# Optimization experiments

Hardware: AMD Instinct MI355X
Metric: run time of the kernel (lower is better)

Reference implementation:

```python
import jax, jax.numpy as jnp
import numpy as np

NT, NV, ND, NM, NP = 50000, 1000, 20000, 5000, 8000
E = 100000
D, H, C = 256, 4, 64          # gnn_hidden_dim, heads, per-head channels
TS_FEAT, EMB, L = 64, 128, 2
NEG_SLOPE = 0.2

SIZES = {'ts': NT, 'vital': NV, 'diag': ND, 'med': NM, 'proc': NP}
EDGE_TYPES = [('ts', 'vital'), ('vital', 'ts'), ('ts', 'diag'), ('diag', 'ts'),
              ('ts', 'med'), ('med', 'ts'), ('ts', 'proc'), ('proc', 'ts')]
T = len(EDGE_TYPES)


def setup_inputs():
    key = jax.random.key(0)
    ks = jax.random.split(key, 32)
    def nrm(k, shape, s=0.05):
        return jax.random.normal(k, shape, dtype=jnp.float32) * s
    inp = {}
    inp['ts_x'] = nrm(ks[0], (NT, TS_FEAT), 1.0)
    inp['emb_vital'] = nrm(ks[1], (NV, EMB), 1.0)
    inp['emb_diag'] = nrm(ks[2], (ND, EMB), 1.0)
    inp['emb_med'] = nrm(ks[3], (NM, EMB), 1.0)
    inp['emb_proc'] = nrm(ks[4], (NP, EMB), 1.0)
    inp['Wp_ts'] = nrm(ks[5], (TS_FEAT, D)); inp['bp_ts'] = jnp.zeros((D,), jnp.float32)
    inp['Wp_c'] = nrm(ks[6], (4, EMB, D)); inp['bp_c'] = jnp.zeros((4, D), jnp.float32)
    inp['Wsrc'] = nrm(ks[7], (L, T, D, H * C))
    inp['Wdst'] = nrm(ks[8], (L, T, D, H * C))
    inp['asrc'] = nrm(ks[9], (L, T, H, C))
    inp['adst'] = nrm(ks[10], (L, T, H, C))
    inp['bconv'] = jnp.zeros((L, T, H * C), jnp.float32)
    inp['Wc1'] = nrm(ks[11], (D, D // 2)); inp['bc1'] = jnp.zeros((D // 2,), jnp.float32)
    inp['Wc2'] = nrm(ks[12], (D // 2, 1)); inp['bc2'] = jnp.zeros((1,), jnp.float32)
    names = ['ei_tv', 'ei_vt', 'ei_td', 'ei_dt', 'ei_tm', 'ei_mt', 'ei_tp', 'ei_pt']
    for i, ((s, d), nm) in enumerate(zip(EDGE_TYPES, names)):
        k1, k2 = jax.random.split(ks[13 + i])
        src = jax.random.randint(k1, (E,), 0, SIZES[s], dtype=jnp.int32)
        dst = jax.random.randint(k2, (E,), 0, SIZES[d], dtype=jnp.int32)
        inp[nm] = jnp.stack([src, dst])
    return inp


def gat_conv(xs, xd, Ws, Wd, a_s, a_d, b, ei, nd):
    """Bipartite PyG GATConv: add_self_loops=False, concat heads, eval (no dropout)."""
    hs = (xs @ Ws).reshape(-1, H, C)            # [Ns,H,C]
    hd = (xd @ Wd).reshape(-1, H, C)            # [Nd,H,C]
    es = jnp.sum(hs * a_s, axis=-1)             # [Ns,H]
    ed = jnp.sum(hd * a_d, axis=-1)             # [Nd,H]
    src, dst = ei[0], ei[1]
    e = jax.nn.leaky_relu(es[src] + ed[dst], NEG_SLOPE)   # [E,H]
    m = jax.ops.segment_max(e, dst, num_segments=nd)      # segment softmax over dst
    ex = jnp.exp(e - m[dst])
    den = jax.ops.segment_sum(ex, dst, num_segments=nd)
    alpha = ex / (den[dst] + 1e-16)
    msg = (alpha[:, :, None] * hs[src]).reshape(-1, H * C)  # [E,H*C]
    return jax.ops.segment_sum(msg, dst, num_segments=nd) + b


def _forward(ts_x, emb_vital, emb_diag, emb_med, emb_proc, Wp_ts, bp_ts, Wp_c, bp_c,
             Wsrc, Wdst, asrc, adst, bconv, Wc1, bc1, Wc2, bc2, edges):
    x = {'ts': ts_x @ Wp_ts + bp_ts,
         'vital': emb_vital @ Wp_c[0] + bp_c[0],
         'diag': emb_diag @ Wp_c[1] + bp_c[1],
         'med': emb_med @ Wp_c[2] + bp_c[2],
         'proc': emb_proc @ Wp_c[3] + bp_c[3]}
    for l in range(L):
        new = {k: jnp.zeros((SIZES[k], D), jnp.float32) for k in x}  # HeteroConv aggr='sum'
        for t, ((s, d), ei) in enumerate(zip(EDGE_TYPES, edges)):
            new[d] = new[d] + gat_conv(x[s], x[d], Wsrc[l, t], Wdst[l, t],
                                       asrc[l, t], adst[l, t], bconv[l, t], ei, SIZES[d])
        x = {k: jax.nn.relu(v) for k, v in new.items()}
    g = jnp.mean(x['ts'], axis=0)               # graph embedding
    h = jax.nn.relu(g @ Wc1 + bc1)
    logits = h @ Wc2 + bc2
    return jnp.squeeze(logits, -1)              # output_classes == 1 -> scalar


def reference(ts_x, emb_vital, emb_diag, emb_med, emb_proc, Wp_ts, bp_ts, Wp_c, bp_c,
              Wsrc, Wdst, asrc, adst, bconv, Wc1, bc1, Wc2, bc2,
              ei_tv, ei_vt, ei_td, ei_dt, ei_tm, ei_mt, ei_tp, ei_pt):
    edges = (ei_tv, ei_vt, ei_td, ei_dt, ei_tm, ei_mt, ei_tp, ei_pt)
    return _forward(ts_x, emb_vital, emb_diag, emb_med, emb_proc, Wp_ts, bp_ts, Wp_c, bp_c,
                    Wsrc, Wdst, asrc, adst, bconv, Wc1, bc1, Wc2, bc2, edges)
```

## Files before the change

kernel.cpp:

```cpp
#include <hip/hip_runtime.h>

#define E_N 100000
#define NTOT 84000
#define NDST 234000

typedef __attribute__((ext_vector_type(8))) short bfrag8;
typedef __attribute__((ext_vector_type(4))) float accf4;

__device__ __forceinline__ void atomAddF(float* p, float v) {
    unsafeAtomicAdd(p, v);
}

__device__ __forceinline__ float lrelu(float v) { return v >= 0.f ? v : 0.2f * v; }

__device__ __forceinline__ unsigned short f2bf(float f) {
    unsigned u = __float_as_uint(f);
    return (unsigned short)((u + 0x7FFFu + ((u >> 16) & 1u)) >> 16);
}
__device__ __forceinline__ float bf2f(unsigned short h) {
    return __uint_as_float(((unsigned)h) << 16);
}

__constant__ int c_tbase[8] = {0, 1000, 51000, 71000, 121000, 126000, 176000, 184000};

struct EI8 { const int* p[8]; };

struct BTJob { const float* W; unsigned short* hi; unsigned short* lo; int K; int kshift; };
struct BTBatch { BTJob j[17]; };

__global__ __launch_bounds__(256) void makeBT(BTBatch b)
{
    BTJob jb = b.j[blockIdx.z];
    int idx = blockIdx.x * 256 + threadIdx.x;
    if (idx >= (jb.K << 8)) return;
    int n = idx >> jb.kshift;
    int k = idx & (jb.K - 1);
    float w = jb.W[(size_t)k * 256 + n];
    unsigned short h = f2bf(w);
    jb.hi[idx] = h;
    jb.lo[idx] = f2bf(w - bf2f(h));
}

struct MJob { const float* A; const unsigned short* BThi; const unsigned short* BTlo;
              float* C; unsigned short* Cbf; const float* bias; int M; int K; int relu; };
struct MBatch { MJob j[8]; };

__global__ __launch_bounds__(256, 2) void gemm_mfma(MBatch batch)
{
    const MJob jb = batch.j[blockIdx.z];
    const int bm = blockIdx.x * 128;
    if (bm >= jb.M) return;
    const int bn = blockIdx.y * 128;
    const int M = jb.M, K = jb.K;

    __shared__ unsigned short Ah[128 * 40];
    __shared__ unsigned short Al[128 * 40];
    __shared__ unsigned short B1[128 * 40];
    __shared__ unsigned short B2[128 * 40];

    const int tid  = threadIdx.x;
    const int wv   = tid >> 6;
    const int lane = tid & 63;
    const int qr = wv >> 1, qc = wv & 1;
    const int lm = lane & 15;
    const int lq = lane >> 4;

    accf4 acc[4][4] = {};

    for (int k0 = 0; k0 < K; k0 += 32) {
#pragma unroll
        for (int it = 0; it < 4; ++it) {
            int slot = it * 256 + tid;
            int m  = slot >> 3;
            int kq = (slot & 7) << 2;
            float4 v = make_float4(0.f, 0.f, 0.f, 0.f);
            if (bm + m < M) v = *(const float4*)(jb.A + (size_t)(bm + m) * K + k0 + kq);
            int o = m * 40 + kq;
            unsigned short h0 = f2bf(v.x), h1 = f2bf(v.y), h2 = f2bf(v.z), h3 = f2bf(v.w);
            Ah[o + 0] = h0; Ah[o + 1] = h1; Ah[o + 2] = h2; Ah[o + 3] = h3;
            Al[o + 0] = f2bf(v.x - bf2f(h0));
            Al[o + 1] = f2bf(v.y - bf2f(h1));
            Al[o + 2] = f2bf(v.z - bf2f(h2));
            Al[o + 3] = f2bf(v.w - bf2f(h3));
        }
#pragma unroll
        for (int it = 0; it < 2; ++it) {
            int slot = it * 256 + tid;
            int n  = slot >> 2;
            int kq = (slot & 3) << 3;
            size_t go = (size_t)(bn + n) * K + k0 + kq;
            *(uint4*)&B1[n * 40 + kq] = *(const uint4*)(jb.BThi + go);
            *(uint4*)&B2[n * 40 + kq] = *(const uint4*)(jb.BTlo + go);
        }
        __syncthreads();

        bfrag8 ah[4], al[4], b1[4], b2[4];
#pragma unroll
        for (int t = 0; t < 4; ++t) {
            int am  = qr * 64 + t * 16 + lm;
            int bnn = qc * 64 + t * 16 + lm;
            ah[t] = *(const bfrag8*)&Ah[am * 40 + lq * 8];
            al[t] = *(const bfrag8*)&Al[am * 40 + lq * 8];
            b1[t] = *(const bfrag8*)&B1[bnn * 40 + lq * 8];
            b2[t] = *(const bfrag8*)&B2[bnn * 40 + lq * 8];
        }
#pragma unroll
        for (int mt = 0; mt < 4; ++mt)
#pragma unroll
            for (int nt = 0; nt < 4; ++nt) {
                acc[mt][nt] = __builtin_amdgcn_mfma_f32_16x16x32_bf16(ah[mt], b1[nt], acc[mt][nt], 0, 0, 0);
                acc[mt][nt] = __builtin_amdgcn_mfma_f32_16x16x32_bf16(al[mt], b1[nt], acc[mt][nt], 0, 0, 0);
                acc[mt][nt] = __builtin_amdgcn_mfma_f32_16x16x32_bf16(ah[mt], b2[nt], acc[mt][nt], 0, 0, 0);
            }
        __syncthreads();
    }

#pragma unroll
    for (int nt = 0; nt < 4; ++nt) {
        int col = bn + qc * 64 + nt * 16 + lm;
        float bv = jb.bias ? jb.bias[col] : 0.f;
#pragma unroll
        for (int mt = 0; mt < 4; ++mt) {
            int row0 = bm + qr * 64 + mt * 16 + lq * 4;
#pragma unroll
            for (int r = 0; r < 4; ++r) {
                int row = row0 + r;
                if (row < M) {
                    float o = acc[mt][nt][r] + bv;
                    if (jb.relu) o = fmaxf(o, 0.f);
                    if (jb.C)   jb.C[(size_t)row * 256 + col] = o;
                    if (jb.Cbf) jb.Cbf[(size_t)row * 256 + col] = f2bf(o);
                }
            }
        }
    }
}

__global__ __launch_bounds__(256) void fill_weff(const float* __restrict__ Wsrc,
                                                 const float* __restrict__ Wdst,
                                                 const float* __restrict__ asrc,
                                                 const float* __restrict__ adst,
                                                 float* __restrict__ weff)
{
    int idx = blockIdx.x * 256 + threadIdx.x;
    if (idx >= 81920) return;
    int col = idx & 31;
    int k   = (idx >> 5) & 255;
    int lnt = idx >> 13;
    int nt  = lnt % 5;
    int l   = lnt / 5;
    bool is_src; int t, h;
    if (nt == 0) {
        if (col < 16) { is_src = true;  t = (col >> 2) * 2;            h = col & 3; }
        else          { is_src = false; t = ((col - 16) >> 2) * 2 + 1; h = col & 3; }
    } else {
        if (col < 4)      { is_src = true;  t = 2 * nt - 1; h = col; }
        else if (col < 8) { is_src = false; t = 2 * nt - 2; h = col - 4; }
        else { weff[idx] = 0.f; return; }
    }
    const float* W = (is_src ? Wsrc : Wdst) + ((size_t)((l * 8 + t) * 256 + k)) * 256 + h * 64;
    const float* a = (is_src ? asrc : adst) + ((size_t)((l * 8 + t) * 4 + h)) * 64;
    float val = 0.f;
    for (int c = 0; c < 64; c++) val += W[c] * a[c];
    weff[idx] = val;
}

template<int NO>
__device__ __forceinline__ void attnproj_body(const float* __restrict__ xrow,
                                              const float* __restrict__ W,
                                              float* __restrict__ out)
{
    float acc[NO];
#pragma unroll
    for (int j = 0; j < NO; j++) acc[j] = 0.f;
    for (int k = 0; k < 256; k += 4) {
        const float4 xv = *(const float4*)(xrow + k);
#pragma unroll
        for (int j = 0; j < NO; j++) {
            acc[j] += xv.x * W[(k + 0) * 32 + j] + xv.y * W[(k + 1) * 32 + j]
                    + xv.z * W[(k + 2) * 32 + j] + xv.w * W[(k + 3) * 32 + j];
        }
    }
#pragma unroll
    for (int j = 0; j < NO; j++) out[j] = acc[j];
}

__global__ __launch_bounds__(256) void attnproj(const float* __restrict__ x,
                                                const float* __restrict__ weff_l,
                                                float* __restrict__ attnT,
                                                float* __restrict__ attnC)
{
    int n = blockIdx.x * 256 + threadIdx.x;
    if (n >= NTOT) return;
    if (n < 50000) {
        attnproj_body<32>(x + (size_t)n * 256, weff_l, attnT + (size_t)n * 32);
    } else {
        int nt = (n < 51000) ? 1 : (n < 71000) ? 2 : (n < 76000) ? 3 : 4;
        attnproj_body<8>(x + (size_t)n * 256, weff_l + nt * 8192, attnC + (size_t)(n - 50000) * 8);
    }
}

__global__ __launch_bounds__(256) void count_k(EI8 ei, int* __restrict__ cnt)
{
    int g = blockIdx.x * 256 + threadIdx.x;
    if (g >= 8 * E_N) return;
    int t = g / E_N;
    int i = g - t * E_N;
    int d = ei.p[t][E_N + i];
    atomicAdd(&cnt[c_tbase[t] + d], 1);
}

__global__ __launch_bounds__(256) void scanA(const int* __restrict__ cnt,
                                             int* __restrict__ rowptr,
                                             int* __restrict__ bsum)
{
    __shared__ int sd[256];
    int b = blockIdx.x, t = threadIdx.x;
    int base = b * 1024 + t * 4;
    int v0 = 0, v1 = 0, v2 = 0, v3 = 0;
    if (base + 0 < NDST) v0 = cnt[base + 0];
    if (base + 1 < NDST) v1 = cnt[base + 1];
    if (base + 2 < NDST) v2 = cnt[base + 2];
    if (base + 3 < NDST) v3 = cnt[base + 3];
    int s = v0 + v1 + v2 + v3;
    sd[t] = s;
    __syncthreads();
    for (int off = 1; off < 256; off <<= 1) {
        int x = 0;
        if (t >= off) x = sd[t - off];
        __syncthreads();
        if (t >= off) sd[t] += x;
        __syncthreads();
    }
    int run = sd[t] - s;
    if (t == 255) bsum[b] = sd[255];
    if (base + 0 < NDST) rowptr[base + 0] = run;          run += v0;
    if (base + 1 < NDST) rowptr[base + 1] = run;          run += v1;
    if (base + 2 < NDST) rowptr[base + 2] = run;          run += v2;
    if (base + 3 < NDST) rowptr[base + 3] = run;
}

__global__ __launch_bounds__(256) void scanB(int* __restrict__ bsum, int nb)
{
    __shared__ int sd[256];
    int t = threadIdx.x;
    int v = (t < nb) ? bsum[t] : 0;
    sd[t] = v;
    __syncthreads();
    for (int off = 1; off < 256; off <<= 1) {
        int x = 0;
        if (t >= off) x = sd[t - off];
        __syncthreads();
        if (t >= off) sd[t] += x;
        __syncthreads();
    }
    if (t < nb) bsum[t] = sd[t] - v;
}

__global__ __launch_bounds__(256) void scanC(int* __restrict__ rowptr,
                                             const int* __restrict__ bsum,
                                             int* __restrict__ cursor)
{
    int b = blockIdx.x, t = threadIdx.x;
    int off = bsum[b];
    int base = b * 1024 + t * 4;
#pragma unroll
    for (int j = 0; j < 4; j++) {
        int i = base + j;
        if (i < NDST) {
            int r = rowptr[i] + off;
            rowptr[i] = r;
            cursor[i] = r;
        }
    }
    if (b == 0 && t == 0) rowptr[NDST] = 8 * E_N;
}

__global__ __launch_bounds__(256) void place_k(EI8 ei, int* __restrict__ cursor,
                                               int* __restrict__ ssrc)
{
    int g = blockIdx.x * 256 + threadIdx.x;
    if (g >= 8 * E_N) return;
    int t = g / E_N;
    int i = g - t * E_N;
    int d = ei.p[t][E_N + i];
    int s = ei.p[t][i];
    int pos = atomicAdd(&cursor[c_tbase[t] + d], 1);
    ssrc[pos] = s;
}

__global__ __launch_bounds__(256) void aggx_k(const float* __restrict__ attnT,
                                              const float* __restrict__ attnC,
                                              const unsigned short* __restrict__ xtsbf,
                                              const int* __restrict__ rowptr,
                                              const int* __restrict__ ssrc,
                                              float* __restrict__ aggx)
{
    int w = blockIdx.x * 4 + (threadIdx.x >> 6);
    int lane = threadIdx.x & 63;
    int h = lane >> 4;
    int ch = (h << 6) | ((lane & 15) << 2);
    int q, dloc;
    if (w < 1000)       { q = 0; dloc = w; }
    else if (w < 21000) { q = 1; dloc = w - 1000; }
    else if (w < 26000) { q = 2; dloc = w - 21000; }
    else                { q = 3; dloc = w - 26000; }
    const int csr4[4]  = {0, 51000, 121000, 176000};
    const int soff4[4] = {0, 4, 8, 12};
    int soff = soff4[q];
    int r0 = rowptr[csr4[q] + dloc], r1 = rowptr[csr4[q] + dloc + 1];
    float ed = attnC[(size_t)w * 8 + 4 + h];
    float den = 0.f, sx = 0.f, sy = 0.f, sz = 0.f, sw = 0.f;
    int e = r0;
    for (; e + 4 <= r1; e += 4) {
        int sA = ssrc[e], sB = ssrc[e + 1], sC = ssrc[e + 2], sD = ssrc[e + 3];
        float eA = attnT[(size_t)sA * 32 + soff + h];
        float eB = attnT[(size_t)sB * 32 + soff + h];
        float eC = attnT[(size_t)sC * 32 + soff + h];
        float eD = attnT[(size_t)sD * 32 + soff + h];
        ushort4 rA = *(const ushort4*)(xtsbf + (size_t)sA * 256 + ch);
        ushort4 rB = *(const ushort4*)(xtsbf + (size_t)sB * 256 + ch);
        ushort4 rC = *(const ushort4*)(xtsbf + (size_t)sC * 256 + ch);
        ushort4 rD = *(const ushort4*)(xtsbf + (size_t)sD * 256 + ch);
        float xA = __expf(lrelu(eA + ed));
        float xB = __expf(lrelu(eB + ed));
        float xC = __expf(lrelu(eC + ed));
        float xD = __expf(lrelu(eD + ed));
        den += (xA + xB) + (xC + xD);
        sx += xA * bf2f(rA.x) + xB * bf2f(rB.x) + xC * bf2f(rC.x) + xD * bf2f(rD.x);
        sy += xA * bf2f(rA.y) + xB * bf2f(rB.y) + xC * bf2f(rC.y) + xD * bf2f(rD.y);
        sz += xA * bf2f(rA.z) + xB * bf2f(rB.z) + xC * bf2f(rC.z) + xD * bf2f(rD.z);
        sw += xA * bf2f(rA.w) + xB * bf2f(rB.w) + xC * bf2f(rC.w) + xD * bf2f(rD.w);
    }
    for (; e < r1; e++) {
        int s = ssrc[e];
        float es = attnT[(size_t)s * 32 + soff + h];
        float ex = __expf(lrelu(es + ed));
        den += ex;
        ushort4 rv = *(const ushort4*)(xtsbf + (size_t)s * 256 + ch);
        sx += ex * bf2f(rv.x); sy += ex * bf2f(rv.y);
        sz += ex * bf2f(rv.z); sw += ex * bf2f(rv.w);
    }
    float inv = 1.f / (den + 1e-16f);
    float4 o; o.x = sx * inv; o.y = sy * inv; o.z = sz * inv; o.w = sw * inv;
    *(float4*)(aggx + (size_t)w * 256 + ch) = o;
}

__global__ __launch_bounds__(256) void agg_ts(const float* __restrict__ attnT,
                                              const float* __restrict__ attnC,
                                              const unsigned short* __restrict__ hscbf,
                                              const int* __restrict__ rowptr,
                                              const int* __restrict__ ssrc,
                                              const float* __restrict__ bconv_l,
                                              float* __restrict__ xout)
{
    int d = blockIdx.x * 4 + (threadIdx.x >> 6);
    int lane = threadIdx.x & 63;
    int h = lane >> 4;
    int ch = (h << 6) | ((lane & 15) << 2);
    const int co4[4]   = {0, 1000, 21000, 26000};
    const int tb4[4]   = {1000, 71000, 126000, 184000};
    const int doff4[4] = {16, 20, 24, 28};
    const int bo4[4]   = {256, 768, 1280, 1792};

    int r0q[4], nq[4]; float edq[4];
    int mx = 0;
#pragma unroll
    for (int q = 0; q < 4; q++) {
        int a = rowptr[tb4[q] + d], b = rowptr[tb4[q] + d + 1];
        r0q[q] = a; nq[q] = b - a;
        mx = max(mx, b - a);
        edq[q] = attnT[(size_t)d * 32 + doff4[q] + h];
    }
    float den[4] = {0.f, 0.f, 0.f, 0.f};
    float sx[4] = {0.f, 0.f, 0.f, 0.f}, sy[4] = {0.f, 0.f, 0.f, 0.f};
    float sz[4] = {0.f, 0.f, 0.f, 0.f}, sw[4] = {0.f, 0.f, 0.f, 0.f};
    for (int i = 0; i < mx; i++) {
#pragma unroll
        for (int q = 0; q < 4; q++) {
            if (i < nq[q]) {
                int s = ssrc[r0q[q] + i];
                float es = attnC[(size_t)(co4[q] + s) * 8 + h];
                float ex = __expf(lrelu(es + edq[q]));
                den[q] += ex;
                ushort4 hv = *(const ushort4*)(hscbf + (size_t)(co4[q] + s) * 256 + ch);
                sx[q] += ex * bf2f(hv.x); sy[q] += ex * bf2f(hv.y);
                sz[q] += ex * bf2f(hv.z); sw[q] += ex * bf2f(hv.w);
            }
        }
    }
    float ax = 0.f, ay = 0.f, az = 0.f, aw = 0.f;
#pragma unroll
    for (int q = 0; q < 4; q++) {
        const float* b = bconv_l + bo4[q] + ch;
        float inv = 1.f / (den[q] + 1e-16f);
        ax += b[0] + sx[q] * inv; ay += b[1] + sy[q] * inv;
        az += b[2] + sz[q] * inv; aw += b[3] + sw[q] * inv;
    }
    float4 o;
    o.x = fmaxf(ax, 0.f); o.y = fmaxf(ay, 0.f);
    o.z = fmaxf(az, 0.f); o.w = fmaxf(aw, 0.f);
    *(float4*)(xout + (size_t)d * 256 + ch) = o;
}

__global__ __launch_bounds__(256) void colsum_ts(const float* __restrict__ x,
                                                 float* __restrict__ gsum)
{
    int c = threadIdx.x;
    float s = 0.f;
    for (int r = blockIdx.x; r < 50000; r += gridDim.x) s += x[(size_t)r * 256 + c];
    atomAddF(gsum + c, s);
}

__global__ __launch_bounds__(128) void head_k(const float* __restrict__ gsum,
                                              const float* __restrict__ Wc1,
                                              const float* __restrict__ bc1,
                                              const float* __restrict__ Wc2,
                                              const float* __restrict__ bc2,
                                              float* __restrict__ out)
{
    __shared__ float g[256];
    __shared__ float red[128];
    int t = threadIdx.x;
    g[t] = gsum[t] * (1.f / 50000.f);
    g[t + 128] = gsum[t + 128] * (1.f / 50000.f);
    __syncthreads();
    float acc = bc1[t];
    for (int k = 0; k < 256; k++) acc += g[k] * Wc1[k * 128 + t];
    red[t] = fmaxf(acc, 0.f) * Wc2[t];
    __syncthreads();
    for (int sft = 64; sft > 0; sft >>= 1) {
        if (t < sft) red[t] += red[t + sft];
        __syncthreads();
    }
    if (t == 0) out[0] = red[0] + bc2[0];
}

extern "C" void kernel_launch(void* const* d_in, const int* in_sizes, int n_in,
                              void* d_out, int out_size, void* d_ws, size_t ws_size,
                              hipStream_t stream)
{
    const float* ts_x   = (const float*)d_in[0];
    const float* emb[4] = {(const float*)d_in[1], (const float*)d_in[2],
                           (const float*)d_in[3], (const float*)d_in[4]};
    const float* Wp_ts  = (const float*)d_in[5];
    const float* bp_ts  = (const float*)d_in[6];
    const float* Wp_c   = (const float*)d_in[7];
    const float* bp_c   = (const float*)d_in[8];
    const float* Wsrc   = (const float*)d_in[9];
    const float* Wdst   = (const float*)d_in[10];
    const float* asrc   = (const float*)d_in[11];
    const float* adst   = (const float*)d_in[12];
    const float* bconv  = (const float*)d_in[13];
    const float* Wc1    = (const float*)d_in[14];
    const float* bc1    = (const float*)d_in[15];
    const float* Wc2    = (const float*)d_in[16];
    const float* bc2    = (const float*)d_in[17];
    EI8 ei;
    for (int t = 0; t < 8; t++) ei.p[t] = (const int*)d_in[18 + t];

    float* x0    = (float*)d_ws;
    float* x1    = x0    + 21504000;
    float* attnT = x1    + 21504000;
    float* attnC = attnT + 1600000;
    float* weff  = attnC + 272000;
    float* gsum  = weff  + 81920;
    int* rowptr  = (int*)(gsum + 256);
    int* bsum    = rowptr + 234004;
    int* ssrc    = bsum + 256;
    unsigned short* xtsbf = (unsigned short*)(ssrc + 800000);
    unsigned short* hscbf = xtsbf + 12800000;
    unsigned short* btp   = hscbf + 8704000;
    int* cursor  = (int*)hscbf;
    float* aggx  = x1;

    unsigned short* bt_ts_h = btp;
    unsigned short* bt_ts_l = bt_ts_h + 16384;
    unsigned short* bt_c_h[4], *bt_c_l[4];
    {
        unsigned short* p = bt_ts_l + 16384;
        for (int q = 0; q < 4; q++) { bt_c_h[q] = p; p += 32768; bt_c_l[q] = p; p += 32768; }
    }
    unsigned short* bt_w = bt_ts_l + 16384 + 8 * 32768;
    auto wpan_h = [&](int l, int t) { return bt_w + (size_t)((l == 0 ? t : 8 + t / 2) * 2) * 65536; };
    auto wpan_l = [&](int l, int t) { return wpan_h(l, t) + 65536; };

    hipMemsetAsync(cursor, 0, NDST * sizeof(int), stream);
    count_k<<<3125, 256, 0, stream>>>(ei, cursor);
    scanA<<<229, 256, 0, stream>>>(cursor, rowptr, bsum);
    scanB<<<1, 256, 0, stream>>>(bsum, 229);
    scanC<<<229, 256, 0, stream>>>(rowptr, bsum, cursor);
    place_k<<<3125, 256, 0, stream>>>(ei, cursor, ssrc);

    {
        BTBatch b = {};
        int zi = 0;
        b.j[zi++] = {Wp_ts, bt_ts_h, bt_ts_l, 64, 6};
        for (int q = 0; q < 4; q++)
            b.j[zi++] = {Wp_c + q * 32768, bt_c_h[q], bt_c_l[q], 128, 7};
        for (int t = 0; t < 8; t++)
            b.j[zi++] = {Wsrc + (size_t)(0 * 8 + t) * 65536, wpan_h(0, t), wpan_l(0, t), 256, 8};
        for (int t = 1; t < 8; t += 2)
            b.j[zi++] = {Wsrc + (size_t)(1 * 8 + t) * 65536, wpan_h(1, t), wpan_l(1, t), 256, 8};
        makeBT<<<dim3(256, 1, 17), 256, 0, stream>>>(b);
    }

    fill_weff<<<320, 256, 0, stream>>>(Wsrc, Wdst, asrc, adst, weff);

    static const int Nd4[4]    = {1000, 20000, 5000, 8000};
    static const int co4[4]    = {0, 1000, 21000, 26000};
    static const int dbase4[4] = {50000, 51000, 71000, 76000};
    static const int tsrc[4]   = {1, 3, 5, 7};
    static const int tdst[4]   = {0, 2, 4, 6};

    {
        MBatch b = {};
        b.j[0] = {ts_x, bt_ts_h, bt_ts_l, x0, xtsbf, bp_ts, 50000, 64, 0};
        for (int q = 0; q < 4; q++)
            b.j[1 + q] = {emb[q], bt_c_h[q], bt_c_l[q], x0 + (size_t)dbase4[q] * 256,
                          nullptr, bp_c + q * 256, Nd4[q], 128, 0};
        gemm_mfma<<<dim3(391, 2, 5), 256, 0, stream>>>(b);
    }

    attnproj<<<329, 256, 0, stream>>>(x0, weff, attnT, attnC);
    aggx_k<<<8500, 256, 0, stream>>>(attnT, attnC, xtsbf, rowptr, ssrc, aggx);
    {
        MBatch b = {};
        for (int q = 0; q < 4; q++)
            b.j[q] = {x0 + (size_t)dbase4[q] * 256, wpan_h(0, tsrc[q]), wpan_l(0, tsrc[q]),
                      nullptr, hscbf + (size_t)co4[q] * 256, nullptr, Nd4[q], 256, 0};
        for (int q = 0; q < 4; q++)
            b.j[4 + q] = {aggx + (size_t)co4[q] * 256, wpan_h(0, tdst[q]), wpan_l(0, tdst[q]),
                          x1 + (size_t)dbase4[q] * 256, nullptr, bconv + tdst[q] * 256, Nd4[q], 256, 1};
        gemm_mfma<<<dim3(157, 2, 8), 256, 0, stream>>>(b);
    }
    agg_ts<<<12500, 256, 0, stream>>>(attnT, attnC, hscbf, rowptr, ssrc, bconv, x1);

    attnproj<<<329, 256, 0, stream>>>(x1, weff + 40960, attnT, attnC);
    {
        MBatch b = {};
        for (int q = 0; q < 4; q++)
            b.j[q] = {x1 + (size_t)dbase4[q] * 256, wpan_h(1, tsrc[q]), wpan_l(1, tsrc[q]),
                      nullptr, hscbf + (size_t)co4[q] * 256, nullptr, Nd4[q], 256, 0};
        gemm_mfma<<<dim3(157, 2, 4), 256, 0, stream>>>(b);
    }
    agg_ts<<<12500, 256, 0, stream>>>(attnT, attnC, hscbf, rowptr, ssrc, bconv + 2048, x0);

    hipMemsetAsync(gsum, 0, 256 * sizeof(float), stream);
    colsum_ts<<<256, 256, 0, stream>>>(x0, gsum);
    head_k<<<1, 128, 0, stream>>>(gsum, Wc1, bc1, Wc2, bc2, (float*)d_out);
}
```

Measured before the change: 756.7 us.

## Store activations as packed hi/lo bf16, swizzle GEMM LDS, fuse final aggregation with column sum

Activations are now stored as packed hi/lo bf16 pairs in 32-bit words, so GEMMs reading them skip the per-tile fp32 split and conversion. The GEMM LDS layout drops the padding in favour of an XOR swizzle, which frees shared memory, and occupancy is raised to 4 blocks per SM. The last-layer ts aggregation is fused with the column mean reduction, so the 50000x256 output is never written and re-read. The packed format keeps roughly fp32 precision but adds pack/unpack ALU work, and the fused kernel serializes 8 destinations per wave with fewer blocks.

```diff
diff --git a/kernel.cpp b/kernel.cpp
--- a/kernel.cpp
+++ b/kernel.cpp
@@ -19,6 +19,14 @@
 }
 __device__ __forceinline__ float bf2f(unsigned short h) {
     return __uint_as_float(((unsigned)h) << 16);
+}
+__device__ __forceinline__ unsigned packf(float o) {
+    unsigned short h = f2bf(o);
+    unsigned short l = f2bf(o - bf2f(h));
+    return (unsigned)h | ((unsigned)l << 16);
+}
+__device__ __forceinline__ float unpk(unsigned u) {
+    return __uint_as_float(u << 16) + __uint_as_float(u & 0xffff0000u);
 }
 
 __constant__ int c_tbase[8] = {0, 1000, 51000, 71000, 121000, 126000, 176000, 184000};
@@ -41,11 +49,11 @@
     jb.lo[idx] = f2bf(w - bf2f(h));
 }
 
-struct MJob { const float* A; const unsigned short* BThi; const unsigned short* BTlo;
-              float* C; unsigned short* Cbf; const float* bias; int M; int K; int relu; };
+struct MJob { const void* A; const unsigned short* BThi; const unsigned short* BTlo;
+              unsigned* Cp; unsigned short* Cbf; const float* bias; int M; int K; int relu; int af32; };
 struct MBatch { MJob j[8]; };
 
-__global__ __launch_bounds__(256, 2) void gemm_mfma(MBatch batch)
+__global__ __launch_bounds__(256, 4) void gemm_mfma(MBatch batch)
 {
     const MJob jb = batch.j[blockIdx.z];
     const int bm = blockIdx.x * 128;
@@ -53,10 +61,10 @@
     const int bn = blockIdx.y * 128;
     const int M = jb.M, K = jb.K;
 
-    __shared__ unsigned short Ah[128 * 40];
-    __shared__ unsigned short Al[128 * 40];
-    __shared__ unsigned short B1[128 * 40];
-    __shared__ unsigned short B2[128 * 40];
+    __shared__ unsigned short Ah[128 * 32];
+    __shared__ unsigned short Al[128 * 32];
+    __shared__ unsigned short B1[128 * 32];
+    __shared__ unsigned short B2[128 * 32];
 
     const int tid  = threadIdx.x;
     const int wv   = tid >> 6;
@@ -73,24 +81,39 @@
             int slot = it * 256 + tid;
             int m  = slot >> 3;
             int kq = (slot & 7) << 2;
-            float4 v = make_float4(0.f, 0.f, 0.f, 0.f);
-            if (bm + m < M) v = *(const float4*)(jb.A + (size_t)(bm + m) * K + k0 + kq);
-            int o = m * 40 + kq;
-            unsigned short h0 = f2bf(v.x), h1 = f2bf(v.y), h2 = f2bf(v.z), h3 = f2bf(v.w);
-            Ah[o + 0] = h0; Ah[o + 1] = h1; Ah[o + 2] = h2; Ah[o + 3] = h3;
-            Al[o + 0] = f2bf(v.x - bf2f(h0));
-            Al[o + 1] = f2bf(v.y - bf2f(h1));
-            Al[o + 2] = f2bf(v.z - bf2f(h2));
-            Al[o + 3] = f2bf(v.w - bf2f(h3));
+            unsigned h01, h23, l01, l23;
+            if (jb.af32) {
+                float4 v = make_float4(0.f, 0.f, 0.f, 0.f);
+                if (bm + m < M) v = *(const float4*)((const float*)jb.A + (size_t)(bm + m) * K + k0 + kq);
+                unsigned short h0 = f2bf(v.x), h1 = f2bf(v.y), h2 = f2bf(v.z), h3 = f2bf(v.w);
+                unsigned short l0 = f2bf(v.x - bf2f(h0)), l1 = f2bf(v.y - bf2f(h1));
+                unsigned short l2 = f2bf(v.z - bf2f(h2)), l3 = f2bf(v.w - bf2f(h3));
+                h01 = (unsigned)h0 | ((unsigned)h1 << 16); h23 = (unsigned)h2 | ((unsigned)h3 << 16);
+                l01 = (unsigned)l0 | ((unsigned)l1 << 16); l23 = (unsigned)l2 | ((unsigned)l3 << 16);
+            } else {
+                uint4 v = make_uint4(0u, 0u, 0u, 0u);
+                if (bm + m < M) v = *(const uint4*)((const unsigned*)jb.A + (size_t)(bm + m) * K + k0 + kq);
+                h01 = (v.x & 0xffffu) | (v.y << 16);
+                h23 = (v.z & 0xffffu) | (v.w << 16);
+                l01 = (v.x >> 16) | (v.y & 0xffff0000u);
+                l23 = (v.z >> 16) | (v.w & 0xffff0000u);
+            }
+            int g = kq >> 3, half = (kq >> 2) & 1;
+            int off = m * 32 + ((g ^ (m & 3)) << 3) + half * 4;
+            uint2 hw; hw.x = h01; hw.y = h23;
+            uint2 lw; lw.x = l01; lw.y = l23;
+            *(uint2*)&Ah[off] = hw;
+            *(uint2*)&Al[off] = lw;
         }
 #pragma unroll
         for (int it = 0; it < 2; ++it) {
             int slot = it * 256 + tid;
-            int n  = slot >> 2;
-            int kq = (slot & 3) << 3;
-            size_t go = (size_t)(bn + n) * K + k0 + kq;
-            *(uint4*)&B1[n * 40 + kq] = *(const uint4*)(jb.BThi + go);
-            *(uint4*)&B2[n * 40 + kq] = *(const uint4*)(jb.BTlo + go);
+            int n = slot >> 2;
+            int g = slot & 3;
+            size_t go = (size_t)(bn + n) * K + k0 + g * 8;
+            int off = n * 32 + ((g ^ (n & 3)) << 3);
+            *(uint4*)&B1[off] = *(const uint4*)(jb.BThi + go);
+            *(uint4*)&B2[off] = *(const uint4*)(jb.BTlo + go);
         }
         __syncthreads();
 
@@ -99,10 +122,10 @@
         for (int t = 0; t < 4; ++t) {
             int am  = qr * 64 + t * 16 + lm;
             int bnn = qc * 64 + t * 16 + lm;
-            ah[t] = *(const bfrag8*)&Ah[am * 40 + lq * 8];
-            al[t] = *(const bfrag8*)&Al[am * 40 + lq * 8];
-            b1[t] = *(const bfrag8*)&B1[bnn * 40 + lq * 8];
-            b2[t] = *(const bfrag8*)&B2[bnn * 40 + lq * 8];
+            ah[t] = *(const bfrag8*)&Ah[am * 32 + ((lq ^ (am & 3)) << 3)];
+            al[t] = *(const bfrag8*)&Al[am * 32 + ((lq ^ (am & 3)) << 3)];
+            b1[t] = *(const bfrag8*)&B1[bnn * 32 + ((lq ^ (bnn & 3)) << 3)];
+            b2[t] = *(const bfrag8*)&B2[bnn * 32 + ((lq ^ (bnn & 3)) << 3)];
         }
 #pragma unroll
         for (int mt = 0; mt < 4; ++mt)
@@ -128,7 +151,7 @@
                 if (row < M) {
                     float o = acc[mt][nt][r] + bv;
                     if (jb.relu) o = fmaxf(o, 0.f);
-                    if (jb.C)   jb.C[(size_t)row * 256 + col] = o;
+                    if (jb.Cp)  jb.Cp[(size_t)row * 256 + col] = packf(o);
                     if (jb.Cbf) jb.Cbf[(size_t)row * 256 + col] = f2bf(o);
                 }
             }
@@ -166,7 +189,7 @@
 }
 
 template<int NO>
-__device__ __forceinline__ void attnproj_body(const float* __restrict__ xrow,
+__device__ __forceinline__ void attnproj_body(const unsigned* __restrict__ xrow,
                                               const float* __restrict__ W,
                                               float* __restrict__ out)
 {
@@ -174,18 +197,19 @@
 #pragma unroll
     for (int j = 0; j < NO; j++) acc[j] = 0.f;
     for (int k = 0; k < 256; k += 4) {
-        const float4 xv = *(const float4*)(xrow + k);
+        const uint4 xv = *(const uint4*)(xrow + k);
+        float x0 = unpk(xv.x), x1 = unpk(xv.y), x2 = unpk(xv.z), x3 = unpk(xv.w);
 #pragma unroll
         for (int j = 0; j < NO; j++) {
-            acc[j] += xv.x * W[(k + 0) * 32 + j] + xv.y * W[(k + 1) * 32 + j]
-                    + xv.z * W[(k + 2) * 32 + j] + xv.w * W[(k + 3) * 32 + j];
+            acc[j] += x0 * W[(k + 0) * 32 + j] + x1 * W[(k + 1) * 32 + j]
+                    + x2 * W[(k + 2) * 32 + j] + x3 * W[(k + 3) * 32 + j];
         }
     }
 #pragma unroll
     for (int j = 0; j < NO; j++) out[j] = acc[j];
 }
 
-__global__ __launch_bounds__(256) void attnproj(const float* __restrict__ x,
+__global__ __launch_bounds__(256) void attnproj(const unsigned* __restrict__ x,
                                                 const float* __restrict__ weff_l,
                                                 float* __restrict__ attnT,
                                                 float* __restrict__ attnC)
@@ -294,7 +318,7 @@
                                               const unsigned short* __restrict__ xtsbf,
                                               const int* __restrict__ rowptr,
                                               const int* __restrict__ ssrc,
-                                              float* __restrict__ aggx)
+                                              unsigned* __restrict__ aggx)
 {
     int w = blockIdx.x * 4 + (threadIdx.x >> 6);
     int lane = threadIdx.x & 63;
@@ -342,8 +366,10 @@
         sz += ex * bf2f(rv.z); sw += ex * bf2f(rv.w);
     }
     float inv = 1.f / (den + 1e-16f);
-    float4 o; o.x = sx * inv; o.y = sy * inv; o.z = sz * inv; o.w = sw * inv;
-    *(float4*)(aggx + (size_t)w * 256 + ch) = o;
+    uint4 o;
+    o.x = packf(sx * inv); o.y = packf(sy * inv);
+    o.z = packf(sz * inv); o.w = packf(sw * inv);
+    *(uint4*)(aggx + (size_t)w * 256 + ch) = o;
 }
 
 __global__ __launch_bounds__(256) void agg_ts(const float* __restrict__ attnT,
@@ -352,7 +378,7 @@
                                               const int* __restrict__ rowptr,
                                               const int* __restrict__ ssrc,
                                               const float* __restrict__ bconv_l,
-                                              float* __restrict__ xout)
+                                              unsigned* __restrict__ xout)
 {
     int d = blockIdx.x * 4 + (threadIdx.x >> 6);
     int lane = threadIdx.x & 63;
@@ -397,19 +423,83 @@
         ax += b[0] + sx[q] * inv; ay += b[1] + sy[q] * inv;
         az += b[2] + sz[q] * inv; aw += b[3] + sw[q] * inv;
     }
-    float4 o;
-    o.x = fmaxf(ax, 0.f); o.y = fmaxf(ay, 0.f);
-    o.z = fmaxf(az, 0.f); o.w = fmaxf(aw, 0.f);
-    *(float4*)(xout + (size_t)d * 256 + ch) = o;
-}
-
-__global__ __launch_bounds__(256) void colsum_ts(const float* __restrict__ x,
-                                                 float* __restrict__ gsum)
-{
-    int c = threadIdx.x;
-    float s = 0.f;
-    for (int r = blockIdx.x; r < 50000; r += gridDim.x) s += x[(size_t)r * 256 + c];
-    atomAddF(gsum + c, s);
+    uint4 o;
+    o.x = packf(fmaxf(ax, 0.f)); o.y = packf(fmaxf(ay, 0.f));
+    o.z = packf(fmaxf(az, 0.f)); o.w = packf(fmaxf(aw, 0.f));
+    *(uint4*)(xout + (size_t)d * 256 + ch) = o;
+}
+
+__global__ __launch_bounds__(256) void agg_tsum(const float* __restrict__ attnT,
+                                                const float* __restrict__ attnC,
+                                                const unsigned short* __restrict__ hscbf,
+                                                const int* __restrict__ rowptr,
+                                                const int* __restrict__ ssrc,
+                                                const float* __restrict__ bconv_l,
+                                                float* __restrict__ gsum)
+{
+    int wv = threadIdx.x >> 6, lane = threadIdx.x & 63;
+    int h = lane >> 4;
+    int ch = (h << 6) | ((lane & 15) << 2);
+    const int co4[4]   = {0, 1000, 21000, 26000};
+    const int tb4[4]   = {1000, 71000, 126000, 184000};
+    const int doff4[4] = {16, 20, 24, 28};
+    const int bo4[4]   = {256, 768, 1280, 1792};
+    float cs0 = 0.f, cs1 = 0.f, cs2 = 0.f, cs3 = 0.f;
+
+    for (int i8 = 0; i8 < 8; ++i8) {
+        int d = (blockIdx.x * 4 + wv) * 8 + i8;
+        if (d >= 50000) break;
+        int r0q[4], nq[4]; float edq[4];
+        int mx = 0;
+#pragma unroll
+        for (int q = 0; q < 4; q++) {
+            int a = rowptr[tb4[q] + d], b = rowptr[tb4[q] + d + 1];
+            r0q[q] = a; nq[q] = b - a;
+            mx = max(mx, b - a);
+            edq[q] = attnT[(size_t)d * 32 + doff4[q] + h];
+        }
+        float den[4] = {0.f, 0.f, 0.f, 0.f};
+        float sx[4] = {0.f, 0.f, 0.f, 0.f}, sy[4] = {0.f, 0.f, 0.f, 0.f};
+        float sz[4] = {0.f, 0.f, 0.f, 0.f}, sw[4] = {0.f, 0.f, 0.f, 0.f};
+        for (int i = 0; i < mx; i++) {
+#pragma unroll
+            for (int q = 0; q < 4; q++) {
+                if (i < nq[q]) {
+                    int s = ssrc[r0q[q] + i];
+                    float es = attnC[(size_t)(co4[q] + s) * 8 + h];
+                    float ex = __expf(lrelu(es + edq[q]));
+                    den[q] += ex;
+                    ushort4 hv = *(const ushort4*)(hscbf + (size_t)(co4[q] + s) * 256 + ch);
+                    sx[q] += ex * bf2f(hv.x); sy[q] += ex * bf2f(hv.y);
+                    sz[q] += ex * bf2f(hv.z); sw[q] += ex * bf2f(hv.w);
+                }
+            }
+        }
+        float ax = 0.f, ay = 0.f, az = 0.f, aw = 0.f;
+#pragma unroll
+        for (int q = 0; q < 4; q++) {
+            const float* b = bconv_l + bo4[q] + ch;
+            float inv = 1.f / (den[q] + 1e-16f);
+            ax += b[0] + sx[q] * inv; ay += b[1] + sy[q] * inv;
+            az += b[2] + sz[q] * inv; aw += b[3] + sw[q] * inv;
+        }
+        cs0 += fmaxf(ax, 0.f); cs1 += fmaxf(ay, 0.f);
+        cs2 += fmaxf(az, 0.f); cs3 += fmaxf(aw, 0.f);
+    }
+
+    __shared__ float4 red4[256];
+    float4 cv; cv.x = cs0; cv.y = cs1; cv.z = cs2; cv.w = cs3;
+    red4[threadIdx.x] = cv;
+    __syncthreads();
+    if (threadIdx.x < 64) {
+        float4 a = red4[threadIdx.x], b = red4[threadIdx.x + 64];
+        float4 c = red4[threadIdx.x + 128], dd = red4[threadIdx.x + 192];
+        int cch = ((threadIdx.x >> 4) << 6) | ((threadIdx.x & 15) << 2);
+        atomAddF(gsum + cch + 0, a.x + b.x + c.x + dd.x);
+        atomAddF(gsum + cch + 1, a.y + b.y + c.y + dd.y);
+        atomAddF(gsum + cch + 2, a.z + b.z + c.z + dd.z);
+        atomAddF(gsum + cch + 3, a.w + b.w + c.w + dd.w);
+    }
 }
 
 __global__ __launch_bounds__(128) void head_k(const float* __restrict__ gsum,
@@ -459,9 +549,9 @@
     EI8 ei;
     for (int t = 0; t < 8; t++) ei.p[t] = (const int*)d_in[18 + t];
 
-    float* x0    = (float*)d_ws;
-    float* x1    = x0    + 21504000;
-    float* attnT = x1    + 21504000;
+    unsigned* x0p  = (unsigned*)d_ws;
+    unsigned* x1p  = x0p  + 21504000;
+    float* attnT = (float*)(x1p + 21504000);
     float* attnC = attnT + 1600000;
     float* weff  = attnC + 272000;
     float* gsum  = weff  + 81920;
@@ -472,7 +562,7 @@
     unsigned short* hscbf = xtsbf + 12800000;
     unsigned short* btp   = hscbf + 8704000;
     int* cursor  = (int*)hscbf;
-    float* aggx  = x1;
+    unsigned* aggx = x1p;
 
     unsigned short* bt_ts_h = btp;
     unsigned short* bt_ts_l = bt_ts_h + 16384;
@@ -515,38 +605,37 @@
 
     {
         MBatch b = {};
-        b.j[0] = {ts_x, bt_ts_h, bt_ts_l, x0, xtsbf, bp_ts, 50000, 64, 0};
+        b.j[0] = {ts_x, bt_ts_h, bt_ts_l, x0p, xtsbf, bp_ts, 50000, 64, 0, 1};
         for (int q = 0; q < 4; q++)
-            b.j[1 + q] = {emb[q], bt_c_h[q], bt_c_l[q], x0 + (size_t)dbase4[q] * 256,
-                          nullptr, bp_c + q * 256, Nd4[q], 128, 0};
+            b.j[1 + q] = {emb[q], bt_c_h[q], bt_c_l[q], x0p + (size_t)dbase4[q] * 256,
+                          nullptr, bp_c + q * 256, Nd4[q], 128, 0, 1};
         gemm_mfma<<<dim3(391, 2, 5), 256, 0, stream>>>(b);
     }
 
-    attnproj<<<329, 256, 0, stream>>>(x0, weff, attnT, attnC);
+    attnproj<<<329, 256, 0, stream>>>(x0p, weff, attnT, attnC);
     aggx_k<<<8500, 256, 0, stream>>>(attnT, attnC, xtsbf, rowptr, ssrc, aggx);
     {
         MBatch b = {};
         for (int q = 0; q < 4; q++)
-            b.j[q] = {x0 + (size_t)dbase4[q] * 256, wpan_h(0, tsrc[q]), wpan_l(0, tsrc[q]),
-                      nullptr, hscbf + (size_t)co4[q] * 256, nullptr, Nd4[q], 256, 0};
+            b.j[q] = {x0p + (size_t)dbase4[q] * 256, wpan_h(0, tsrc[q]), wpan_l(0, tsrc[q]),
+                      nullptr, hscbf + (size_t)co4[q] * 256, nullptr, Nd4[q], 256, 0, 0};
         for (int q = 0; q < 4; q++)
             b.j[4 + q] = {aggx + (size_t)co4[q] * 256, wpan_h(0, tdst[q]), wpan_l(0, tdst[q]),
-                          x1 + (size_t)dbase4[q] * 256, nullptr, bconv + tdst[q] * 256, Nd4[q], 256, 1};
+                          x1p + (size_t)dbase4[q] * 256, nullptr, bconv + tdst[q] * 256, Nd4[q], 256, 1, 0};
         gemm_mfma<<<dim3(157, 2, 8), 256, 0, stream>>>(b);
     }
-    agg_ts<<<12500, 256, 0, stream>>>(attnT, attnC, hscbf, rowptr, ssrc, bconv, x1);
-
-    attnproj<<<329, 256, 0, stream>>>(x1, weff + 40960, attnT, attnC);
+    agg_ts<<<12500, 256, 0, stream>>>(attnT, attnC, hscbf, rowptr, ssrc, bconv, x1p);
+
+    attnproj<<<329, 256, 0, stream>>>(x1p, weff + 40960, attnT, attnC);
     {
         MBatch b = {};
         for (int q = 0; q < 4; q++)
-            b.j[q] = {x1 + (size_t)dbase4[q] * 256, wpan_h(1, tsrc[q]), wpan_l(1, tsrc[q]),
-                      nullptr, hscbf + (size_t)co4[q] * 256, nullptr, Nd4[q], 256, 0};
+            b.j[q] = {x1p + (size_t)dbase4[q] * 256, wpan_h(1, tsrc[q]), wpan_l(1, tsrc[q]),
+                      nullptr, hscbf + (size_t)co4[q] * 256, nullptr, Nd4[q], 256, 0, 0};
         gemm_mfma<<<dim3(157, 2, 4), 256, 0, stream>>>(b);
     }
-    agg_ts<<<12500, 256, 0, stream>>>(attnT, attnC, hscbf, rowptr, ssrc, bconv + 2048, x0);
-
     hipMemsetAsync(gsum, 0, 256 * sizeof(float), stream);
-    colsum_ts<<<256, 256, 0, stream>>>(x0, gsum);
+    agg_tsum<<<1563, 256, 0, stream>>>(attnT, attnC, hscbf, rowptr, ssrc, bconv + 2048, gsum);
+
     head_k<<<1, 128, 0, stream>>>(gsum, Wc1, bc1, Wc2, bc2, (float*)d_out);
 }
```

Result: slower. 957.7 us (+26.6%).

## Fuse final ts aggregation with mean-pool partials and swizzle GEMM block order

Applied to the files above, without the earlier changes.

The last ts aggregation kernel now reduces its four destination rows per block in shared memory and writes per-block partial column sums, so the full 50000x256 layer-2 output is never written and re-read by the column-sum kernel. The GEMM grid is flattened to one dimension and remapped so the two 128-wide column halves of a row block run on adjacent blocks in groups of eight, which should improve L2 reuse of the A tile. The partial buffer reuses x0, and the remap has to cover every row block for each job size.

```diff
diff --git a/kernel.cpp b/kernel.cpp
--- a/kernel.cpp
+++ b/kernel.cpp
@@ -48,9 +48,12 @@
 __global__ __launch_bounds__(256, 2) void gemm_mfma(MBatch batch)
 {
     const MJob jb = batch.j[blockIdx.z];
-    const int bm = blockIdx.x * 128;
+    const int bx = blockIdx.x;
+    const int rowblk = (bx >> 4) * 8 + (bx & 7);
+    const int half = (bx >> 3) & 1;
+    const int bm = rowblk * 128;
     if (bm >= jb.M) return;
-    const int bn = blockIdx.y * 128;
+    const int bn = half * 128;
     const int M = jb.M, K = jb.K;
 
     __shared__ unsigned short Ah[128 * 40];
@@ -346,23 +349,18 @@
     *(float4*)(aggx + (size_t)w * 256 + ch) = o;
 }
 
-__global__ __launch_bounds__(256) void agg_ts(const float* __restrict__ attnT,
+__device__ __forceinline__ float4 agg_ts_core(const float* __restrict__ attnT,
                                               const float* __restrict__ attnC,
                                               const unsigned short* __restrict__ hscbf,
                                               const int* __restrict__ rowptr,
                                               const int* __restrict__ ssrc,
                                               const float* __restrict__ bconv_l,
-                                              float* __restrict__ xout)
-{
-    int d = blockIdx.x * 4 + (threadIdx.x >> 6);
-    int lane = threadIdx.x & 63;
-    int h = lane >> 4;
-    int ch = (h << 6) | ((lane & 15) << 2);
+                                              int d, int h, int ch)
+{
     const int co4[4]   = {0, 1000, 21000, 26000};
     const int tb4[4]   = {1000, 71000, 126000, 184000};
     const int doff4[4] = {16, 20, 24, 28};
     const int bo4[4]   = {256, 768, 1280, 1792};
-
     int r0q[4], nq[4]; float edq[4];
     int mx = 0;
 #pragma unroll
@@ -400,15 +398,60 @@
     float4 o;
     o.x = fmaxf(ax, 0.f); o.y = fmaxf(ay, 0.f);
     o.z = fmaxf(az, 0.f); o.w = fmaxf(aw, 0.f);
+    return o;
+}
+
+__global__ __launch_bounds__(256) void agg_ts(const float* __restrict__ attnT,
+                                              const float* __restrict__ attnC,
+                                              const unsigned short* __restrict__ hscbf,
+                                              const int* __restrict__ rowptr,
+                                              const int* __restrict__ ssrc,
+                                              const float* __restrict__ bconv_l,
+                                              float* __restrict__ xout)
+{
+    int d = blockIdx.x * 4 + (threadIdx.x >> 6);
+    int lane = threadIdx.x & 63;
+    int h = lane >> 4;
+    int ch = (h << 6) | ((lane & 15) << 2);
+    float4 o = agg_ts_core(attnT, attnC, hscbf, rowptr, ssrc, bconv_l, d, h, ch);
     *(float4*)(xout + (size_t)d * 256 + ch) = o;
 }
 
-__global__ __launch_bounds__(256) void colsum_ts(const float* __restrict__ x,
-                                                 float* __restrict__ gsum)
+__global__ __launch_bounds__(256) void agg_ts_pool(const float* __restrict__ attnT,
+                                                   const float* __restrict__ attnC,
+                                                   const unsigned short* __restrict__ hscbf,
+                                                   const int* __restrict__ rowptr,
+                                                   const int* __restrict__ ssrc,
+                                                   const float* __restrict__ bconv_l,
+                                                   float* __restrict__ part)
+{
+    int d = blockIdx.x * 4 + (threadIdx.x >> 6);
+    int lane = threadIdx.x & 63;
+    int h = lane >> 4;
+    int ch = (h << 6) | ((lane & 15) << 2);
+    float4 o = agg_ts_core(attnT, attnC, hscbf, rowptr, ssrc, bconv_l, d, h, ch);
+    __shared__ float4 red4[256];
+    red4[threadIdx.x] = o;
+    __syncthreads();
+    if (threadIdx.x < 64) {
+        float4 a = red4[threadIdx.x], b = red4[threadIdx.x + 64];
+        float4 c = red4[threadIdx.x + 128], dd = red4[threadIdx.x + 192];
+        float4 s;
+        s.x = (a.x + b.x) + (c.x + dd.x);
+        s.y = (a.y + b.y) + (c.y + dd.y);
+        s.z = (a.z + b.z) + (c.z + dd.z);
+        s.w = (a.w + b.w) + (c.w + dd.w);
+        int cch = ((threadIdx.x >> 4) << 6) | ((threadIdx.x & 15) << 2);
+        *(float4*)(part + (size_t)blockIdx.x * 256 + cch) = s;
+    }
+}
+
+__global__ __launch_bounds__(256) void colsum_part(const float* __restrict__ part,
+                                                   float* __restrict__ gsum)
 {
     int c = threadIdx.x;
     float s = 0.f;
-    for (int r = blockIdx.x; r < 50000; r += gridDim.x) s += x[(size_t)r * 256 + c];
+    for (int r = blockIdx.x; r < 12500; r += gridDim.x) s += part[(size_t)r * 256 + c];
     atomAddF(gsum + c, s);
 }
 
@@ -473,6 +516,7 @@
     unsigned short* btp   = hscbf + 8704000;
     int* cursor  = (int*)hscbf;
     float* aggx  = x1;
+    float* part  = x0;
 
     unsigned short* bt_ts_h = btp;
     unsigned short* bt_ts_l = bt_ts_h + 16384;
@@ -519,7 +563,7 @@
         for (int q = 0; q < 4; q++)
             b.j[1 + q] = {emb[q], bt_c_h[q], bt_c_l[q], x0 + (size_t)dbase4[q] * 256,
                           nullptr, bp_c + q * 256, Nd4[q], 128, 0};
-        gemm_mfma<<<dim3(391, 2, 5), 256, 0, stream>>>(b);
+        gemm_mfma<<<dim3(784, 1, 5), 256, 0, stream>>>(b);
     }
 
     attnproj<<<329, 256, 0, stream>>>(x0, weff, attnT, attnC);
@@ -532,7 +576,7 @@
         for (int q = 0; q < 4; q++)
             b.j[4 + q] = {aggx + (size_t)co4[q] * 256, wpan_h(0, tdst[q]), wpan_l(0, tdst[q]),
                           x1 + (size_t)dbase4[q] * 256, nullptr, bconv + tdst[q] * 256, Nd4[q], 256, 1};
-        gemm_mfma<<<dim3(157, 2, 8), 256, 0, stream>>>(b);
+        gemm_mfma<<<dim3(320, 1, 8), 256, 0, stream>>>(b);
     }
     agg_ts<<<12500, 256, 0, stream>>>(attnT, attnC, hscbf, rowptr, ssrc, bconv, x1);
 
@@ -542,11 +586,11 @@
         for (int q = 0; q < 4; q++)
             b.j[q] = {x1 + (size_t)dbase4[q] * 256, wpan_h(1, tsrc[q]), wpan_l(1, tsrc[q]),
                       nullptr, hscbf + (size_t)co4[q] * 256, nullptr, Nd4[q], 256, 0};
-        gemm_mfma<<<dim3(157, 2, 4), 256, 0, stream>>>(b);
-    }
-    agg_ts<<<12500, 256, 0, stream>>>(attnT, attnC, hscbf, rowptr, ssrc, bconv + 2048, x0);
-
+        gemm_mfma<<<dim3(320, 1, 4), 256, 0, stream>>>(b);
+    }
+    agg_ts_pool<<<12500, 256, 0, stream>>>(attnT, attnC, hscbf, rowptr, ssrc, bconv + 2048, part);
     hipMemsetAsync(gsum, 0, 256 * sizeof(float), stream);
-    colsum_ts<<<256, 256, 0, stream>>>(x0, gsum);
+    colsum_part<<<256, 256, 0, stream>>>(part, gsum);
+
     head_k<<<1, 128, 0, stream>>>(gsum, Wc1, bc1, Wc2, bc2, (float*)d_out);
 }
```

Result: faster. 723.5 us (-4.4%).
